# Optimization experiments

Measured on AMD Instinct MI355X. Metric: run time of the kernel, lower is better.

The kernel has to match this reference:

```python
import jax, jax.numpy as jnp
import numpy as np
from jax import lax

FEAT = 56  # features_size
SR = 2     # sr_ratio
NUM_HEADS = 8

# Constant relative-distance indices, shape (N, N, 2) with values in [0, 2*FEAT-2]
_idx = np.array([[i, j] for i in range(FEAT) for j in range(FEAT)])
REL = jnp.asarray(_idx[None, :, :] - _idx[:, None, :] + FEAT - 1)  # (N, N, 2)


def setup_inputs() -> dict:
    key = jax.random.key(0)
    ks = jax.random.split(key, 8)
    dim = 256
    B = 4
    x = jax.random.normal(ks[0], (B, dim, FEAT, FEAT), dtype=jnp.float32)
    Wq = jax.random.normal(ks[1], (dim, dim), dtype=jnp.float32) * 0.02
    Wkv = jax.random.normal(ks[2], (dim, 2 * dim), dtype=jnp.float32) * 0.02
    sr_w = jax.random.normal(ks[3], (dim, dim, SR, SR), dtype=jnp.float32) * 0.02  # OIHW
    sr_b = jnp.zeros((dim,), dtype=jnp.float32)
    ln_g = jnp.ones((dim,), dtype=jnp.float32)
    ln_b = jnp.zeros((dim,), dtype=jnp.float32)
    pos_emb = jax.random.normal(ks[4], (2 * FEAT - 1, 2 * FEAT - 1), dtype=jnp.float32) * 0.2
    proj_w = jax.random.normal(ks[5], (dim, dim), dtype=jnp.float32) * 0.02
    proj_b = jnp.zeros((dim,), dtype=jnp.float32)
    return {"x": x, "Wq": Wq, "Wkv": Wkv, "sr_w": sr_w, "sr_b": sr_b,
            "ln_g": ln_g, "ln_b": ln_b, "pos_emb": pos_emb,
            "proj_w": proj_w, "proj_b": proj_b}


def reference(x, Wq, Wkv, sr_w, sr_b, ln_g, ln_b, pos_emb, proj_w, proj_b):
    B, C, H, W = x.shape
    N = H * W
    h = NUM_HEADS
    hd = C // h
    scale = hd ** -0.5

    x_q = x.reshape(B, C, N).transpose(0, 2, 1)            # (B, N, C)
    q = (x_q @ Wq).reshape(B, N, h, hd).transpose(0, 2, 1, 3)  # (B, h, N, hd)

    # spatial reduction conv (kernel=stride=SR) + layernorm
    xr = lax.conv_general_dilated(x, sr_w, (SR, SR), 'VALID',
                                  dimension_numbers=('NCHW', 'OIHW', 'NCHW'))
    xr = xr + sr_b[None, :, None, None]
    Nk = (H // SR) * (W // SR)
    x_kv = xr.reshape(B, C, Nk).transpose(0, 2, 1)          # (B, Nk, C)
    mu = jnp.mean(x_kv, axis=-1, keepdims=True)
    var = jnp.var(x_kv, axis=-1, keepdims=True)
    x_kv = (x_kv - mu) * lax.rsqrt(var + 1e-5) * ln_g + ln_b

    # kv projection; einops '(dim h l)' split: head_dim slowest, l fastest
    kv = (x_kv @ Wkv).reshape(B, Nk, hd, h, 2)
    k = kv[..., 0].transpose(0, 3, 1, 2)                    # (B, h, Nk, hd)
    v = kv[..., 1].transpose(0, 3, 1, 2)                    # (B, h, Nk, hd)

    attn = jnp.einsum('bhnd,bhmd->bhnm', q, k) * scale      # (B, h, N, Nk)
    bias = pos_emb[REL[..., 0], REL[..., 1]][:, :Nk]        # (N, Nk)
    attn = jax.nn.softmax(attn + bias, axis=-1)

    out = jnp.einsum('bhnm,bhmd->bhnd', attn, v)            # (B, h, N, hd)
    out = out.transpose(0, 2, 1, 3).reshape(B, N, C)
    out = out @ proj_w + proj_b
    return out.transpose(0, 2, 1).reshape(B, C, H, W)
```

## Files before the change

### kernel.cpp

```cpp
#include <hip/hip_runtime.h>
#include <hip/hip_bf16.h>

typedef float f32x4 __attribute__((ext_vector_type(4)));
typedef short s16x8 __attribute__((ext_vector_type(8)));
typedef unsigned short u16x4 __attribute__((ext_vector_type(4)));
typedef unsigned short u16x8 __attribute__((ext_vector_type(8)));

#define MFMA16(a,b,c) __builtin_amdgcn_mfma_f32_16x16x32_bf16(a,b,c,0,0,0)

#define NTOK 3136
#define NKV  784
#define NKVP 800
#define CD   256
#define NH   8
#define HD   32
#define PEW  111
#define LOG2E 1.4426950408889634f
#define SC2  (0.17677669529663687f * 1.4426950408889634f)

static __device__ __forceinline__ unsigned short f2b(float f){
  unsigned int u = __float_as_uint(f);
  return (unsigned short)((u + 0x7fffu + ((u>>16)&1u)) >> 16);
}
static __device__ __forceinline__ unsigned short f2b_fast(float f){
  __hip_bfloat16 h = __float2bfloat16(f);
  return *reinterpret_cast<unsigned short*>(&h);
}
static __device__ __forceinline__ float b2f(unsigned short u){
  return __uint_as_float(((unsigned int)u)<<16);
}
static __device__ __forceinline__ void gload16(const unsigned short* g, unsigned short* l){
  __builtin_amdgcn_global_load_lds(
      (const __attribute__((address_space(1))) unsigned int*)g,
      (__attribute__((address_space(3))) unsigned int*)l, 16, 0, 0);
}

__global__ __launch_bounds__(256) void k_prep(
      const float* __restrict__ Wq, const float* __restrict__ Wkv,
      const float* __restrict__ pw, const float* __restrict__ srw,
      const float* __restrict__ pos, const float* __restrict__ x,
      unsigned short* __restrict__ WqT, unsigned short* __restrict__ WkvT,
      unsigned short* __restrict__ pwT, unsigned short* __restrict__ srwb2,
      unsigned short* __restrict__ bias2, unsigned short* __restrict__ xbf,
      unsigned short* __restrict__ kb, unsigned short* __restrict__ vT){
  __shared__ float tile[64][65];
  const int blk = blockIdx.x, t = threadIdx.x;
  if (blk < 2048){
    int i = blk*256 + t;
    if (i < 65536){ int nn=i>>8, kk=i&255; WqT[i] = f2b(Wq[kk*256+nn]); }
    else if (i < 196608){ int j=i-65536; int c2=j>>8, kk=j&255; WkvT[j] = f2b(Wkv[kk*512+c2]); }
    else if (i < 262144){ int j=i-196608; int cc=j>>8, kk=j&255; pwT[j] = f2b(pw[kk*256+cc]); }
    else { int j=i-262144; int o=j>>10, rem=j&1023, khw=rem>>8, ci=rem&255;
           srwb2[j] = f2b(srw[o*1024 + ci*4 + khw]); }
  } else if (blk < 2176){
    int i = (blk-2048)*256 + t;
    if (i < 16384){
      int bh=i>>9, r=i&511, ridx=r>>5, d=r&31;
      int row = 776 + (ridx&7) + (ridx>>3)*16;
      kb[((size_t)bh*NKVP + row)*HD + d] = 0;
    } else {
      int j=i-16384;
      int bh=j>>9, r=j&511, d=r>>4, key=784+(r&15);
      vT[((size_t)bh*HD + d)*NKVP + key] = 0;
    }
  } else if (blk < 5312){
    int n = blk - 2176;
    if (t < 200){
      int nr = (n*9363)>>19, nc = n - nr*56;
      u16x4 o;
#pragma unroll
      for (int j=0;j<4;++j){
        int key = t*4 + j;
        float v;
        if (key < NKV){
          int tt = (key*9363)>>19, mm = key - tt*56;
          v = pos[(tt-nr+55)*PEW + (mm-nc+55)] * LOG2E;
        } else v = -100000.f;
        o[j] = f2b(v);
      }
      *(u16x4*)&bias2[(size_t)n*NKVP + t*4] = o;
    }
  } else {
    int bx = blk - 5312;
    const int n0 = (bx%49)*64; int c4 = bx/49;
    const int c0 = (c4&3)*64, b = c4>>2;
    const int tx = t&15, ty = t>>4;
#pragma unroll
    for (int j=0;j<4;++j){
      f32x4 v = *(const f32x4*)&x[(size_t)(b*CD + c0+ty+j*16)*NTOK + n0 + tx*4];
      tile[ty+j*16][tx*4+0]=v[0]; tile[ty+j*16][tx*4+1]=v[1];
      tile[ty+j*16][tx*4+2]=v[2]; tile[ty+j*16][tx*4+3]=v[3];
    }
    __syncthreads();
    const int nr = t>>2, ccb = (t&3)*16;
    u16x8 o0, o1;
#pragma unroll
    for (int u=0;u<8;++u){ o0[u] = f2b(tile[ccb+u][nr]); o1[u] = f2b(tile[ccb+8+u][nr]); }
    unsigned short* dst = &xbf[((size_t)b*NTOK + n0+nr)*CD + c0 + ccb];
    *(u16x8*)dst = o0;
    *(u16x8*)(dst+8) = o1;
  }
}

__global__ __launch_bounds__(256) void k_qproj(const unsigned short* __restrict__ xbf,
      const unsigned short* __restrict__ WqT, unsigned short* __restrict__ qb){
  const int tid=threadIdx.x, wv=tid>>6, l=tid&63, g=l>>4, ln16=l&15;
  const int bI = blockIdx.x/49;
  const int n0 = (blockIdx.x%49)*64;
  const int m0 = n0 + (wv>>1)*32;
  const int c0 = blockIdx.y*64 + (wv&1)*32;
  const unsigned short* ap0 = &xbf[((size_t)bI*NTOK + m0+ln16)*CD + g*8];
  const unsigned short* ap1 = ap0 + 16*CD;
  const unsigned short* bp0 = &WqT[(size_t)(c0+ln16)*CD + g*8];
  const unsigned short* bp1 = bp0 + 16*CD;
  f32x4 acc[2][2] = {};
  s16x8 a0 = *(const s16x8*)ap0, a1 = *(const s16x8*)ap1;
  s16x8 w0 = *(const s16x8*)bp0, w1 = *(const s16x8*)bp1;
#pragma unroll
  for (int k0=0; k0<CD; k0+=32){
    s16x8 na0 = *(const s16x8*)(ap0 + k0+32);
    s16x8 na1 = *(const s16x8*)(ap1 + k0+32);
    s16x8 nw0 = *(const s16x8*)(bp0 + k0+32);
    s16x8 nw1 = *(const s16x8*)(bp1 + k0+32);
    acc[0][0] = MFMA16(a0, w0, acc[0][0]);
    acc[0][1] = MFMA16(a0, w1, acc[0][1]);
    acc[1][0] = MFMA16(a1, w0, acc[1][0]);
    acc[1][1] = MFMA16(a1, w1, acc[1][1]);
    a0=na0; a1=na1; w0=nw0; w1=nw1;
  }
#pragma unroll
  for (int mi=0;mi<2;++mi)
#pragma unroll
    for (int ni=0;ni<2;++ni){
      int c = c0 + ni*16 + ln16;
#pragma unroll
      for (int r=0;r<4;++r){
        int n = m0 + mi*16 + g*4 + r;
        qb[((size_t)bI*NTOK + n)*CD + c] = f2b(acc[mi][ni][r] * SC2);
      }
    }
}

__global__ __launch_bounds__(256) void k_conv(const unsigned short* __restrict__ xbf,
      const unsigned short* __restrict__ srwb2, const float* __restrict__ srb,
      float* __restrict__ convo){
  const int tid=threadIdx.x, wv=tid>>6, l=tid&63, g=l>>4, ln16=l&15;
  const int m0 = blockIdx.x*64 + (wv>>1)*32;
  const int c0 = blockIdx.y*64 + (wv&1)*32;
  size_t abase[2][4];
#pragma unroll
  for (int mi=0;mi<2;++mi){
    int m = m0 + mi*16 + ln16;
    int bb = (m>=2352)?3:(m>=1568)?2:(m>=784)?1:0;
    int nk = m - bb*784;
    int pp = (nk*9363)>>18, qq = nk - pp*28;
#pragma unroll
    for (int khw=0;khw<4;++khw){
      int kh = khw>>1, kw = khw&1;
      abase[mi][khw] = ((size_t)bb*NTOK + (2*pp+kh)*56 + 2*qq+kw)*CD;
    }
  }
  const unsigned short* wp0 = &srwb2[(size_t)(c0+ln16)*1024 + g*8];
  const unsigned short* wp1 = wp0 + 16*1024;
  f32x4 acc[2][2] = {};
  s16x8 a0 = *(const s16x8*)&xbf[abase[0][0] + g*8];
  s16x8 a1 = *(const s16x8*)&xbf[abase[1][0] + g*8];
  s16x8 w0 = *(const s16x8*)wp0;
  s16x8 w1 = *(const s16x8*)wp1;
#pragma unroll
  for (int s=0; s<32; ++s){
    const int s1 = s+1;
    const int khw2 = (s1>>3)&3, kc2 = (s1&7)*32;
    const int woff = (s1&31)*32;
    s16x8 na0 = *(const s16x8*)&xbf[abase[0][khw2] + kc2 + g*8];
    s16x8 na1 = *(const s16x8*)&xbf[abase[1][khw2] + kc2 + g*8];
    s16x8 nw0 = *(const s16x8*)(wp0 + woff);
    s16x8 nw1 = *(const s16x8*)(wp1 + woff);
    acc[0][0] = MFMA16(a0, w0, acc[0][0]);
    acc[0][1] = MFMA16(a0, w1, acc[0][1]);
    acc[1][0] = MFMA16(a1, w0, acc[1][0]);
    acc[1][1] = MFMA16(a1, w1, acc[1][1]);
    a0=na0; a1=na1; w0=nw0; w1=nw1;
  }
#pragma unroll
  for (int mi=0;mi<2;++mi)
#pragma unroll
    for (int ni=0;ni<2;++ni){
      int c = c0 + ni*16 + ln16;
      float bias = srb[c];
#pragma unroll
      for (int r=0;r<4;++r){
        int m = m0 + mi*16 + g*4 + r;
        convo[(size_t)m*CD + c] = acc[mi][ni][r] + bias;
      }
    }
}

__global__ void k_ln(const float* __restrict__ co, const float* __restrict__ gam,
                     const float* __restrict__ bet, unsigned short* __restrict__ kvbf){
  const int row = blockIdx.x, t = threadIdx.x;
  float v = co[(size_t)row*CD + t];
  float s = v, s2 = v*v;
#pragma unroll
  for (int o=32; o>0; o>>=1){ s += __shfl_down(s,o); s2 += __shfl_down(s2,o); }
  __shared__ float ps[4], ps2[4];
  int wid = t>>6, lane = t&63;
  if (lane==0){ ps[wid]=s; ps2[wid]=s2; }
  __syncthreads();
  if (t==0){
    float a = ps[0]+ps[1]+ps[2]+ps[3];
    float a2 = ps2[0]+ps2[1]+ps2[2]+ps2[3];
    float mu = a*(1.f/CD);
    float var = a2*(1.f/CD) - mu*mu;
    ps[0] = mu; ps2[0] = rsqrtf(var + 1e-5f);
  }
  __syncthreads();
  float mu = ps[0], rs = ps2[0];
  kvbf[(size_t)row*CD + t] = f2b((v-mu)*rs*gam[t] + bet[t]);
}

__global__ __launch_bounds__(256) void k_kv(const unsigned short* __restrict__ kvbf,
      const unsigned short* __restrict__ WkvT, unsigned short* __restrict__ kb,
      unsigned short* __restrict__ vT){
  const int tid=threadIdx.x, wv=tid>>6, l=tid&63, g=l>>4, ln16=l&15;
  const int m0 = blockIdx.x*64 + (wv>>1)*32;
  const int c0 = blockIdx.y*64 + (wv&1)*32;
  const unsigned short* ap0 = &kvbf[(size_t)(m0+ln16)*CD + g*8];
  const unsigned short* ap1 = ap0 + 16*CD;
  const unsigned short* bp0 = &WkvT[(size_t)(c0+ln16)*CD + g*8];
  const unsigned short* bp1 = bp0 + 16*CD;
  f32x4 acc[2][2] = {};
  s16x8 a0 = *(const s16x8*)ap0, a1 = *(const s16x8*)ap1;
  s16x8 w0 = *(const s16x8*)bp0, w1 = *(const s16x8*)bp1;
#pragma unroll
  for (int k0=0; k0<CD; k0+=32){
    s16x8 na0 = *(const s16x8*)(ap0 + k0+32);
    s16x8 na1 = *(const s16x8*)(ap1 + k0+32);
    s16x8 nw0 = *(const s16x8*)(bp0 + k0+32);
    s16x8 nw1 = *(const s16x8*)(bp1 + k0+32);
    acc[0][0] = MFMA16(a0, w0, acc[0][0]);
    acc[0][1] = MFMA16(a0, w1, acc[0][1]);
    acc[1][0] = MFMA16(a1, w0, acc[1][0]);
    acc[1][1] = MFMA16(a1, w1, acc[1][1]);
    a0=na0; a1=na1; w0=nw0; w1=nw1;
  }
#pragma unroll
  for (int mi=0;mi<2;++mi)
#pragma unroll
    for (int ni=0;ni<2;++ni){
      int c2 = c0 + ni*16 + ln16;
      int d = c2>>4, hh = (c2>>1)&7;
#pragma unroll
      for (int r=0;r<4;++r){
        int m = m0 + mi*16 + g*4 + r;
        int bq = (m>=2352)?3:(m>=1568)?2:(m>=784)?1:0;
        int nk = m - bq*784;
        unsigned short val = f2b(acc[mi][ni][r]);
        if (c2&1){
          vT[(((size_t)bq*NH+hh)*HD + d)*NKVP + nk] = val;
        } else {
          int chunk = nk & ~31, pos = nk & 31;
          int gg = pos>>3, jj = pos&7;
          int row = (jj<4) ? (gg*4+jj) : (16 + gg*4 + (jj-4));
          kb[(((size_t)bq*NH+hh)*NKVP + chunk + row)*HD + d] = val;
        }
      }
    }
}

__global__ __launch_bounds__(256) void k_attn(const unsigned short* __restrict__ qb,
      const unsigned short* __restrict__ kb, const unsigned short* __restrict__ vT,
      const unsigned short* __restrict__ bias2, unsigned short* __restrict__ aout){
  __shared__ unsigned short kv0[2048], kv1[2048], kv2[2048];
  const int tid=threadIdx.x, wv=tid>>6, l=tid&63, g=l>>4, ln16=l&15;
  const int bh = blockIdx.x, b = bh>>3, h = bh&7;
  const int nw = blockIdx.y*64 + wv*16;
  const s16x8 qf = *(const s16x8*)&qb[((size_t)b*NTOK + nw + ln16)*CD + h*HD + g*8];
  const unsigned short* kbase = kb + (size_t)bh*NKVP*HD;
  const unsigned short* vbase = vT + (size_t)bh*HD*NKVP;
  const unsigned short* bp = bias2 + (size_t)(nw + ln16)*NKVP + g*8;
  const int lslot = ((l&3)^((l>>3)&3))*8;
  const unsigned short* sp = (wv < 2)
      ? (kbase + (size_t)(wv*16 + (l>>2))*HD + lslot)
      : (vbase + (size_t)((wv-2)*16 + (l>>2))*NKVP + lslot);
  const int sstep = (wv < 2) ? 1024 : 32;
  const int ko0 = ln16*32 + (g ^ ((ln16>>1)&3))*8;
  unsigned short *bA = kv0, *bB = kv1, *bC = kv2;
  f32x4 accO0 = {}, accO1 = {};
  float S = 0.f;
  const f32x4 zf = {};
  gload16(sp,          bA + wv*512);
  u16x8 bb = *(const u16x8*)bp;
  gload16(sp + sstep,  bB + wv*512);
  u16x8 b1 = *(const u16x8*)(bp + 32);
  for (int it=0; it<25; ++it){
    if (it < 23) asm volatile("s_waitcnt vmcnt(2)" ::: "memory");
    else         asm volatile("s_waitcnt vmcnt(0)" ::: "memory");
    __builtin_amdgcn_s_barrier();
    __builtin_amdgcn_sched_barrier(0);
    u16x8 b2 = b1;
    if (it < 23){
      gload16(sp + (it+2)*sstep, bC + wv*512);
      b2 = *(const u16x8*)(bp + (it+2)*32);
    }
    s16x8 ka0 = *(const s16x8*)&bA[ko0];
    s16x8 ka1 = *(const s16x8*)&bA[512 + ko0];
    s16x8 v0  = *(const s16x8*)&bA[1024 + ko0];
    s16x8 v1  = *(const s16x8*)&bA[1536 + ko0];
    __builtin_amdgcn_s_setprio(1);
    f32x4 d0 = MFMA16(ka0, qf, zf);
    f32x4 d1 = MFMA16(ka1, qf, zf);
    float p[8];
#pragma unroll
    for (int r=0;r<4;++r){
      p[r]   = exp2f(d0[r] + b2f(bb[r]));
      p[4+r] = exp2f(d1[r] + b2f(bb[4+r]));
    }
    S += ((p[0]+p[1])+(p[2]+p[3])) + ((p[4]+p[5])+(p[6]+p[7]));
    s16x8 pf;
#pragma unroll
    for (int j=0;j<8;++j) pf[j] = (short)f2b_fast(p[j]);
    accO0 = MFMA16(pf, v0, accO0);
    accO1 = MFMA16(pf, v1, accO1);
    __builtin_amdgcn_s_setprio(0);
    unsigned short* tmp = bA; bA = bB; bB = bC; bC = tmp;
    bb = b1; b1 = b2;
  }
  S += __shfl_xor(S, 16);
  S += __shfl_xor(S, 32);
#pragma unroll
  for (int r=0;r<4;++r){
    float Sr = __shfl(S, g*4 + r);
    float inv = 1.f / Sr;
    int n = nw + g*4 + r;
    aout[((size_t)b*NTOK + n)*CD + h*HD + ln16]      = f2b(accO0[r]*inv);
    aout[((size_t)b*NTOK + n)*CD + h*HD + 16 + ln16] = f2b(accO1[r]*inv);
  }
}

__global__ __launch_bounds__(256) void k_proj(const unsigned short* __restrict__ ain,
      const unsigned short* __restrict__ pwT, const float* __restrict__ pb,
      float* __restrict__ out){
  const int tid=threadIdx.x, wv=tid>>6, l=tid&63, g=l>>4, ln16=l&15;
  const int bI = blockIdx.x/49;
  const int n0 = (blockIdx.x%49)*64;
  const int nsub = n0 + (wv&1)*32;
  const int c0 = blockIdx.y*64 + (wv>>1)*32;
  const unsigned short* ap0 = &pwT[(size_t)(c0+ln16)*CD + g*8];
  const unsigned short* ap1 = ap0 + 16*CD;
  const unsigned short* bp0 = &ain[((size_t)bI*NTOK + nsub+ln16)*CD + g*8];
  const unsigned short* bp1 = bp0 + 16*CD;
  f32x4 acc[2][2] = {};
  s16x8 a0 = *(const s16x8*)ap0, a1 = *(const s16x8*)ap1;
  s16x8 w0 = *(const s16x8*)bp0, w1 = *(const s16x8*)bp1;
#pragma unroll
  for (int k0=0; k0<CD; k0+=32){
    s16x8 na0 = *(const s16x8*)(ap0 + k0+32);
    s16x8 na1 = *(const s16x8*)(ap1 + k0+32);
    s16x8 nw0 = *(const s16x8*)(bp0 + k0+32);
    s16x8 nw1 = *(const s16x8*)(bp1 + k0+32);
    acc[0][0] = MFMA16(a0, w0, acc[0][0]);
    acc[0][1] = MFMA16(a0, w1, acc[0][1]);
    acc[1][0] = MFMA16(a1, w0, acc[1][0]);
    acc[1][1] = MFMA16(a1, w1, acc[1][1]);
    a0=na0; a1=na1; w0=nw0; w1=nw1;
  }
#pragma unroll
  for (int mi=0;mi<2;++mi)
#pragma unroll
    for (int r=0;r<4;++r){
      int c = c0 + mi*16 + g*4 + r;
      float bias = pb[c];
#pragma unroll
      for (int ni=0;ni<2;++ni){
        int n = nsub + ni*16 + ln16;
        out[((size_t)bI*CD + c)*NTOK + n] = acc[mi][ni][r] + bias;
      }
    }
}

extern "C" void kernel_launch(void* const* d_in, const int* in_sizes, int n_in,
                              void* d_out, int out_size, void* d_ws, size_t ws_size,
                              hipStream_t stream){
  const float* x   = (const float*)d_in[0];
  const float* Wq  = (const float*)d_in[1];
  const float* Wkv = (const float*)d_in[2];
  const float* srw = (const float*)d_in[3];
  const float* srb = (const float*)d_in[4];
  const float* lng = (const float*)d_in[5];
  const float* lnb = (const float*)d_in[6];
  const float* pos = (const float*)d_in[7];
  const float* pw  = (const float*)d_in[8];
  const float* pb  = (const float*)d_in[9];
  float* out = (float*)d_out;

  unsigned char* p = (unsigned char*)d_ws;
  unsigned short* WqT   = (unsigned short*)(p + 0);
  unsigned short* WkvT  = (unsigned short*)(p + 131072);
  unsigned short* pwT   = (unsigned short*)(p + 393216);
  unsigned short* srwb2 = (unsigned short*)(p + 524288);
  unsigned short* bias2 = (unsigned short*)(p + 1048576);
  unsigned short* xbf   = (unsigned short*)(p + 6066176);
  unsigned short* qbuf  = (unsigned short*)(p + 12488704);
  float*          convo = (float*)        (p + 18911232);
  unsigned short* kvbf  = (unsigned short*)(p + 22122496);
  unsigned short* kbuf  = (unsigned short*)(p + 23728128);
  unsigned short* vT    = (unsigned short*)(p + 25366528);
  unsigned short* aout  = (unsigned short*)(p + 27004928);

  k_prep <<<6096, 256, 0, stream>>>(Wq, Wkv, pw, srw, pos, x,
                                    WqT, WkvT, pwT, srwb2, bias2, xbf, kbuf, vT);
  k_qproj<<<dim3(196,4), 256, 0, stream>>>(xbf, WqT, qbuf);
  k_conv <<<dim3(49,4),  256, 0, stream>>>(xbf, srwb2, srb, convo);
  k_ln   <<<3136, 256, 0, stream>>>(convo, lng, lnb, kvbf);
  k_kv   <<<dim3(49,8),  256, 0, stream>>>(kvbf, WkvT, kbuf, vT);
  k_attn <<<dim3(32,49), 256, 0, stream>>>(qbuf, kbuf, vT, bias2, aout);
  k_proj <<<dim3(196,4), 256, 0, stream>>>(aout, pwT, pb, out);
}
```

Before: 193.4 us.

## Fuse kernels, tile weight transposes, and process two query tiles per attention block

The Q projection and the spatial-reduction conv now run as one launch sharing a grid. LayerNorm is fused into the KV projection through a swizzled LDS tile, which removes the intermediate bf16 buffer and one launch. Weight transposes in prep go through an LDS-tiled path for coalesced access. The attention kernel handles two 64-row query tiles per block so each staged K/V tile is reused twice, and it packs probabilities to bf16 with a cheaper rounding. The costs are higher register pressure in attention, a masked tail tile, and the LayerNorm now being recomputed by each of the 8 column blocks.

```diff
diff --git a/kernel.cpp b/kernel.cpp
--- a/kernel.cpp
+++ b/kernel.cpp
@@ -22,10 +22,6 @@
   unsigned int u = __float_as_uint(f);
   return (unsigned short)((u + 0x7fffu + ((u>>16)&1u)) >> 16);
 }
-static __device__ __forceinline__ unsigned short f2b_fast(float f){
-  __hip_bfloat16 h = __float2bfloat16(f);
-  return *reinterpret_cast<unsigned short*>(&h);
-}
 static __device__ __forceinline__ float b2f(unsigned short u){
   return __uint_as_float(((unsigned int)u)<<16);
 }
@@ -33,6 +29,18 @@
   __builtin_amdgcn_global_load_lds(
       (const __attribute__((address_space(1))) unsigned int*)g,
       (__attribute__((address_space(3))) unsigned int*)l, 16, 0, 0);
+}
+static __device__ __forceinline__ s16x8 pack8(const float* p){
+  union { uint4 u; s16x8 s; } w;
+  unsigned int a0=__float_as_uint(p[0])+0x8000u, a1=__float_as_uint(p[1])+0x8000u;
+  unsigned int a2=__float_as_uint(p[2])+0x8000u, a3=__float_as_uint(p[3])+0x8000u;
+  unsigned int a4=__float_as_uint(p[4])+0x8000u, a5=__float_as_uint(p[5])+0x8000u;
+  unsigned int a6=__float_as_uint(p[6])+0x8000u, a7=__float_as_uint(p[7])+0x8000u;
+  w.u.x = (a0>>16) | (a1 & 0xFFFF0000u);
+  w.u.y = (a2>>16) | (a3 & 0xFFFF0000u);
+  w.u.z = (a4>>16) | (a5 & 0xFFFF0000u);
+  w.u.w = (a6>>16) | (a7 & 0xFFFF0000u);
+  return w.s;
 }
 
 __global__ __launch_bounds__(256) void k_prep(
@@ -45,15 +53,32 @@
       unsigned short* __restrict__ kb, unsigned short* __restrict__ vT){
   __shared__ float tile[64][65];
   const int blk = blockIdx.x, t = threadIdx.x;
-  if (blk < 2048){
-    int i = blk*256 + t;
-    if (i < 65536){ int nn=i>>8, kk=i&255; WqT[i] = f2b(Wq[kk*256+nn]); }
-    else if (i < 196608){ int j=i-65536; int c2=j>>8, kk=j&255; WkvT[j] = f2b(Wkv[kk*512+c2]); }
-    else if (i < 262144){ int j=i-196608; int cc=j>>8, kk=j&255; pwT[j] = f2b(pw[kk*256+cc]); }
-    else { int j=i-262144; int o=j>>10, rem=j&1023, khw=rem>>8, ci=rem&255;
-           srwb2[j] = f2b(srw[o*1024 + ci*4 + khw]); }
-  } else if (blk < 2176){
-    int i = (blk-2048)*256 + t;
+  const int tx = t&15, ty = t>>4;
+  if (blk < 64){
+    const float* src; unsigned short* dst; int sr0, sc0, sstr;
+    if (blk < 16){ src=Wq; dst=WqT; sstr=256; sr0=(blk>>2)*64; sc0=(blk&3)*64; }
+    else if (blk < 32){ int b2=blk-16; src=pw; dst=pwT; sstr=256; sr0=(b2>>2)*64; sc0=(b2&3)*64; }
+    else { int b2=blk-32; src=Wkv; dst=WkvT; sstr=512; sr0=(b2>>3)*64; sc0=(b2&7)*64; }
+#pragma unroll
+    for (int j=0;j<4;++j){
+      f32x4 v = *(const f32x4*)&src[(size_t)(sr0+ty+j*16)*sstr + sc0 + tx*4];
+      tile[ty+j*16][tx*4+0]=v[0]; tile[ty+j*16][tx*4+1]=v[1];
+      tile[ty+j*16][tx*4+2]=v[2]; tile[ty+j*16][tx*4+3]=v[3];
+    }
+    __syncthreads();
+    const int nr = t>>2, ccb = (t&3)*16;
+    u16x8 o0, o1;
+#pragma unroll
+    for (int u=0;u<8;++u){ o0[u]=f2b(tile[ccb+u][nr]); o1[u]=f2b(tile[ccb+8+u][nr]); }
+    unsigned short* dp = &dst[(size_t)(sc0+nr)*256 + sr0 + ccb];
+    *(u16x8*)dp = o0;
+    *(u16x8*)(dp+8) = o1;
+  } else if (blk < 1088){
+    int j = (blk-64)*256 + t;
+    int o=j>>10, rem=j&1023, khw=rem>>8, ci=rem&255;
+    srwb2[j] = f2b(srw[o*1024 + ci*4 + khw]);
+  } else if (blk < 1216){
+    int i = (blk-1088)*256 + t;
     if (i < 16384){
       int bh=i>>9, r=i&511, ridx=r>>5, d=r&31;
       int row = 776 + (ridx&7) + (ridx>>3)*16;
@@ -63,10 +88,10 @@
       int bh=j>>9, r=j&511, d=r>>4, key=784+(r&15);
       vT[((size_t)bh*HD + d)*NKVP + key] = 0;
     }
-  } else if (blk < 5312){
-    int n = blk - 2176;
+  } else if (blk < 4352){
+    int n = blk - 1216;
     if (t < 200){
-      int nr = (n*9363)>>19, nc = n - nr*56;
+      int nr2 = (n*9363)>>19, nc = n - nr2*56;
       u16x4 o;
 #pragma unroll
       for (int j=0;j<4;++j){
@@ -74,17 +99,16 @@
         float v;
         if (key < NKV){
           int tt = (key*9363)>>19, mm = key - tt*56;
-          v = pos[(tt-nr+55)*PEW + (mm-nc+55)] * LOG2E;
+          v = pos[(tt-nr2+55)*PEW + (mm-nc+55)] * LOG2E;
         } else v = -100000.f;
         o[j] = f2b(v);
       }
       *(u16x4*)&bias2[(size_t)n*NKVP + t*4] = o;
     }
   } else {
-    int bx = blk - 5312;
+    int bx = blk - 4352;
     const int n0 = (bx%49)*64; int c4 = bx/49;
     const int c0 = (c4&3)*64, b = c4>>2;
-    const int tx = t&15, ty = t>>4;
 #pragma unroll
     for (int j=0;j<4;++j){
       f32x4 v = *(const f32x4*)&x[(size_t)(b*CD + c0+ty+j*16)*NTOK + n0 + tx*4];
@@ -95,154 +119,169 @@
     const int nr = t>>2, ccb = (t&3)*16;
     u16x8 o0, o1;
 #pragma unroll
-    for (int u=0;u<8;++u){ o0[u] = f2b(tile[ccb+u][nr]); o1[u] = f2b(tile[ccb+8+u][nr]); }
+    for (int u=0;u<8;++u){ o0[u]=f2b(tile[ccb+u][nr]); o1[u]=f2b(tile[ccb+8+u][nr]); }
     unsigned short* dst = &xbf[((size_t)b*NTOK + n0+nr)*CD + c0 + ccb];
     *(u16x8*)dst = o0;
     *(u16x8*)(dst+8) = o1;
   }
 }
 
-__global__ __launch_bounds__(256) void k_qproj(const unsigned short* __restrict__ xbf,
-      const unsigned short* __restrict__ WqT, unsigned short* __restrict__ qb){
+__global__ __launch_bounds__(256) void k_qc(const unsigned short* __restrict__ xbf,
+      const unsigned short* __restrict__ WqT, const unsigned short* __restrict__ srwb2,
+      const float* __restrict__ srb, unsigned short* __restrict__ qb,
+      float* __restrict__ convo){
+  const int gid = blockIdx.x;
   const int tid=threadIdx.x, wv=tid>>6, l=tid&63, g=l>>4, ln16=l&15;
-  const int bI = blockIdx.x/49;
-  const int n0 = (blockIdx.x%49)*64;
-  const int m0 = n0 + (wv>>1)*32;
+  if (gid < 784){
+    const int bx = gid % 196, by = gid / 196;
+    const int bI = bx/49;
+    const int n0 = (bx%49)*64;
+    const int m0 = n0 + (wv>>1)*32;
+    const int c0 = by*64 + (wv&1)*32;
+    const unsigned short* ap0 = &xbf[((size_t)bI*NTOK + m0+ln16)*CD + g*8];
+    const unsigned short* ap1 = ap0 + 16*CD;
+    const unsigned short* bp0 = &WqT[(size_t)(c0+ln16)*CD + g*8];
+    const unsigned short* bp1 = bp0 + 16*CD;
+    f32x4 acc[2][2] = {};
+    s16x8 a0 = *(const s16x8*)ap0, a1 = *(const s16x8*)ap1;
+    s16x8 w0 = *(const s16x8*)bp0, w1 = *(const s16x8*)bp1;
+#pragma unroll
+    for (int k0=0; k0<CD; k0+=32){
+      s16x8 na0 = *(const s16x8*)(ap0 + k0+32);
+      s16x8 na1 = *(const s16x8*)(ap1 + k0+32);
+      s16x8 nw0 = *(const s16x8*)(bp0 + k0+32);
+      s16x8 nw1 = *(const s16x8*)(bp1 + k0+32);
+      acc[0][0] = MFMA16(a0, w0, acc[0][0]);
+      acc[0][1] = MFMA16(a0, w1, acc[0][1]);
+      acc[1][0] = MFMA16(a1, w0, acc[1][0]);
+      acc[1][1] = MFMA16(a1, w1, acc[1][1]);
+      a0=na0; a1=na1; w0=nw0; w1=nw1;
+    }
+#pragma unroll
+    for (int mi=0;mi<2;++mi)
+#pragma unroll
+      for (int ni=0;ni<2;++ni){
+        int c = c0 + ni*16 + ln16;
+#pragma unroll
+        for (int r=0;r<4;++r){
+          int n = m0 + mi*16 + g*4 + r;
+          qb[((size_t)bI*NTOK + n)*CD + c] = f2b(acc[mi][ni][r] * SC2);
+        }
+      }
+  } else {
+    const int cid = gid - 784;
+    const int m0 = (cid%49)*64 + (wv>>1)*32;
+    const int c0 = (cid/49)*64 + (wv&1)*32;
+    size_t abase[2][4];
+#pragma unroll
+    for (int mi=0;mi<2;++mi){
+      int m = m0 + mi*16 + ln16;
+      int bb = (m>=2352)?3:(m>=1568)?2:(m>=784)?1:0;
+      int nk = m - bb*784;
+      int pp = (nk*9363)>>18, qq = nk - pp*28;
+#pragma unroll
+      for (int khw=0;khw<4;++khw){
+        int kh = khw>>1, kw = khw&1;
+        abase[mi][khw] = ((size_t)bb*NTOK + (2*pp+kh)*56 + 2*qq+kw)*CD;
+      }
+    }
+    const unsigned short* wp0 = &srwb2[(size_t)(c0+ln16)*1024 + g*8];
+    const unsigned short* wp1 = wp0 + 16*1024;
+    f32x4 acc[2][2] = {};
+    s16x8 a0 = *(const s16x8*)&xbf[abase[0][0] + g*8];
+    s16x8 a1 = *(const s16x8*)&xbf[abase[1][0] + g*8];
+    s16x8 w0 = *(const s16x8*)wp0;
+    s16x8 w1 = *(const s16x8*)wp1;
+#pragma unroll
+    for (int s=0; s<32; ++s){
+      const int s1 = s+1;
+      const int khw2 = (s1>>3)&3, kc2 = (s1&7)*32;
+      const int woff = (s1&31)*32;
+      s16x8 na0 = *(const s16x8*)&xbf[abase[0][khw2] + kc2 + g*8];
+      s16x8 na1 = *(const s16x8*)&xbf[abase[1][khw2] + kc2 + g*8];
+      s16x8 nw0 = *(const s16x8*)(wp0 + woff);
+      s16x8 nw1 = *(const s16x8*)(wp1 + woff);
+      acc[0][0] = MFMA16(a0, w0, acc[0][0]);
+      acc[0][1] = MFMA16(a0, w1, acc[0][1]);
+      acc[1][0] = MFMA16(a1, w0, acc[1][0]);
+      acc[1][1] = MFMA16(a1, w1, acc[1][1]);
+      a0=na0; a1=na1; w0=nw0; w1=nw1;
+    }
+#pragma unroll
+    for (int mi=0;mi<2;++mi)
+#pragma unroll
+      for (int ni=0;ni<2;++ni){
+        int c = c0 + ni*16 + ln16;
+        float bias = srb[c];
+#pragma unroll
+        for (int r=0;r<4;++r){
+          int m = m0 + mi*16 + g*4 + r;
+          convo[(size_t)m*CD + c] = acc[mi][ni][r] + bias;
+        }
+      }
+  }
+}
+
+__global__ __launch_bounds__(256) void k_kvln(const float* __restrict__ co,
+      const float* __restrict__ gam, const float* __restrict__ bet,
+      const unsigned short* __restrict__ WkvT, unsigned short* __restrict__ kb,
+      unsigned short* __restrict__ vT){
+  __shared__ unsigned short As[64*256];
+  const int tid=threadIdx.x, wv=tid>>6, l=tid&63, g=l>>4, ln16=l&15;
+  const int m0blk = blockIdx.x*64;
+  {
+    const int rl = tid>>2, cs = (tid&3)*64;
+    const float* src = &co[(size_t)(m0blk+rl)*CD + cs];
+    f32x4 vals[16];
+    float s=0.f, s2=0.f;
+#pragma unroll
+    for (int i=0;i<16;++i){
+      vals[i] = *(const f32x4*)(src + i*4);
+#pragma unroll
+      for (int q=0;q<4;++q){ s += vals[i][q]; s2 += vals[i][q]*vals[i][q]; }
+    }
+    s += __shfl_xor(s,1); s2 += __shfl_xor(s2,1);
+    s += __shfl_xor(s,2); s2 += __shfl_xor(s2,2);
+    float mu = s*(1.f/CD);
+    float rs = rsqrtf(s2*(1.f/CD) - mu*mu + 1e-5f);
+#pragma unroll
+    for (int u=0;u<8;++u){
+      f32x4 g4a = *(const f32x4*)&gam[cs+u*8];
+      f32x4 g4b = *(const f32x4*)&gam[cs+u*8+4];
+      f32x4 b4a = *(const f32x4*)&bet[cs+u*8];
+      f32x4 b4b = *(const f32x4*)&bet[cs+u*8+4];
+      u16x8 o;
+#pragma unroll
+      for (int q=0;q<4;++q){
+        o[q]   = f2b((vals[u*2][q]  -mu)*rs*g4a[q] + b4a[q]);
+        o[4+q] = f2b((vals[u*2+1][q]-mu)*rs*g4b[q] + b4b[q]);
+      }
+      int off = (rl*256 + cs + u*8) ^ ((rl&7)<<3);
+      *(u16x8*)&As[off] = o;
+    }
+  }
+  __syncthreads();
+  const int mw0 = (wv>>1)*32;
   const int c0 = blockIdx.y*64 + (wv&1)*32;
-  const unsigned short* ap0 = &xbf[((size_t)bI*NTOK + m0+ln16)*CD + g*8];
-  const unsigned short* ap1 = ap0 + 16*CD;
-  const unsigned short* bp0 = &WqT[(size_t)(c0+ln16)*CD + g*8];
+  const unsigned short* bp0 = &WkvT[(size_t)(c0+ln16)*CD + g*8];
   const unsigned short* bp1 = bp0 + 16*CD;
   f32x4 acc[2][2] = {};
-  s16x8 a0 = *(const s16x8*)ap0, a1 = *(const s16x8*)ap1;
   s16x8 w0 = *(const s16x8*)bp0, w1 = *(const s16x8*)bp1;
+  const int mr0 = mw0 + ln16, mr1 = mw0 + 16 + ln16;
 #pragma unroll
   for (int k0=0; k0<CD; k0+=32){
-    s16x8 na0 = *(const s16x8*)(ap0 + k0+32);
-    s16x8 na1 = *(const s16x8*)(ap1 + k0+32);
-    s16x8 nw0 = *(const s16x8*)(bp0 + k0+32);
-    s16x8 nw1 = *(const s16x8*)(bp1 + k0+32);
+    s16x8 a0 = *(const s16x8*)&As[(mr0*256 + k0 + g*8) ^ ((mr0&7)<<3)];
+    s16x8 a1 = *(const s16x8*)&As[(mr1*256 + k0 + g*8) ^ ((mr1&7)<<3)];
+    s16x8 nw0 = w0, nw1 = w1;
+    if (k0 < CD-32){
+      nw0 = *(const s16x8*)(bp0 + k0+32);
+      nw1 = *(const s16x8*)(bp1 + k0+32);
+    }
     acc[0][0] = MFMA16(a0, w0, acc[0][0]);
     acc[0][1] = MFMA16(a0, w1, acc[0][1]);
     acc[1][0] = MFMA16(a1, w0, acc[1][0]);
     acc[1][1] = MFMA16(a1, w1, acc[1][1]);
-    a0=na0; a1=na1; w0=nw0; w1=nw1;
-  }
-#pragma unroll
-  for (int mi=0;mi<2;++mi)
-#pragma unroll
-    for (int ni=0;ni<2;++ni){
-      int c = c0 + ni*16 + ln16;
-#pragma unroll
-      for (int r=0;r<4;++r){
-        int n = m0 + mi*16 + g*4 + r;
-        qb[((size_t)bI*NTOK + n)*CD + c] = f2b(acc[mi][ni][r] * SC2);
-      }
-    }
-}
-
-__global__ __launch_bounds__(256) void k_conv(const unsigned short* __restrict__ xbf,
-      const unsigned short* __restrict__ srwb2, const float* __restrict__ srb,
-      float* __restrict__ convo){
-  const int tid=threadIdx.x, wv=tid>>6, l=tid&63, g=l>>4, ln16=l&15;
-  const int m0 = blockIdx.x*64 + (wv>>1)*32;
-  const int c0 = blockIdx.y*64 + (wv&1)*32;
-  size_t abase[2][4];
-#pragma unroll
-  for (int mi=0;mi<2;++mi){
-    int m = m0 + mi*16 + ln16;
-    int bb = (m>=2352)?3:(m>=1568)?2:(m>=784)?1:0;
-    int nk = m - bb*784;
-    int pp = (nk*9363)>>18, qq = nk - pp*28;
-#pragma unroll
-    for (int khw=0;khw<4;++khw){
-      int kh = khw>>1, kw = khw&1;
-      abase[mi][khw] = ((size_t)bb*NTOK + (2*pp+kh)*56 + 2*qq+kw)*CD;
-    }
-  }
-  const unsigned short* wp0 = &srwb2[(size_t)(c0+ln16)*1024 + g*8];
-  const unsigned short* wp1 = wp0 + 16*1024;
-  f32x4 acc[2][2] = {};
-  s16x8 a0 = *(const s16x8*)&xbf[abase[0][0] + g*8];
-  s16x8 a1 = *(const s16x8*)&xbf[abase[1][0] + g*8];
-  s16x8 w0 = *(const s16x8*)wp0;
-  s16x8 w1 = *(const s16x8*)wp1;
-#pragma unroll
-  for (int s=0; s<32; ++s){
-    const int s1 = s+1;
-    const int khw2 = (s1>>3)&3, kc2 = (s1&7)*32;
-    const int woff = (s1&31)*32;
-    s16x8 na0 = *(const s16x8*)&xbf[abase[0][khw2] + kc2 + g*8];
-    s16x8 na1 = *(const s16x8*)&xbf[abase[1][khw2] + kc2 + g*8];
-    s16x8 nw0 = *(const s16x8*)(wp0 + woff);
-    s16x8 nw1 = *(const s16x8*)(wp1 + woff);
-    acc[0][0] = MFMA16(a0, w0, acc[0][0]);
-    acc[0][1] = MFMA16(a0, w1, acc[0][1]);
-    acc[1][0] = MFMA16(a1, w0, acc[1][0]);
-    acc[1][1] = MFMA16(a1, w1, acc[1][1]);
-    a0=na0; a1=na1; w0=nw0; w1=nw1;
-  }
-#pragma unroll
-  for (int mi=0;mi<2;++mi)
-#pragma unroll
-    for (int ni=0;ni<2;++ni){
-      int c = c0 + ni*16 + ln16;
-      float bias = srb[c];
-#pragma unroll
-      for (int r=0;r<4;++r){
-        int m = m0 + mi*16 + g*4 + r;
-        convo[(size_t)m*CD + c] = acc[mi][ni][r] + bias;
-      }
-    }
-}
-
-__global__ void k_ln(const float* __restrict__ co, const float* __restrict__ gam,
-                     const float* __restrict__ bet, unsigned short* __restrict__ kvbf){
-  const int row = blockIdx.x, t = threadIdx.x;
-  float v = co[(size_t)row*CD + t];
-  float s = v, s2 = v*v;
-#pragma unroll
-  for (int o=32; o>0; o>>=1){ s += __shfl_down(s,o); s2 += __shfl_down(s2,o); }
-  __shared__ float ps[4], ps2[4];
-  int wid = t>>6, lane = t&63;
-  if (lane==0){ ps[wid]=s; ps2[wid]=s2; }
-  __syncthreads();
-  if (t==0){
-    float a = ps[0]+ps[1]+ps[2]+ps[3];
-    float a2 = ps2[0]+ps2[1]+ps2[2]+ps2[3];
-    float mu = a*(1.f/CD);
-    float var = a2*(1.f/CD) - mu*mu;
-    ps[0] = mu; ps2[0] = rsqrtf(var + 1e-5f);
-  }
-  __syncthreads();
-  float mu = ps[0], rs = ps2[0];
-  kvbf[(size_t)row*CD + t] = f2b((v-mu)*rs*gam[t] + bet[t]);
-}
-
-__global__ __launch_bounds__(256) void k_kv(const unsigned short* __restrict__ kvbf,
-      const unsigned short* __restrict__ WkvT, unsigned short* __restrict__ kb,
-      unsigned short* __restrict__ vT){
-  const int tid=threadIdx.x, wv=tid>>6, l=tid&63, g=l>>4, ln16=l&15;
-  const int m0 = blockIdx.x*64 + (wv>>1)*32;
-  const int c0 = blockIdx.y*64 + (wv&1)*32;
-  const unsigned short* ap0 = &kvbf[(size_t)(m0+ln16)*CD + g*8];
-  const unsigned short* ap1 = ap0 + 16*CD;
-  const unsigned short* bp0 = &WkvT[(size_t)(c0+ln16)*CD + g*8];
-  const unsigned short* bp1 = bp0 + 16*CD;
-  f32x4 acc[2][2] = {};
-  s16x8 a0 = *(const s16x8*)ap0, a1 = *(const s16x8*)ap1;
-  s16x8 w0 = *(const s16x8*)bp0, w1 = *(const s16x8*)bp1;
-#pragma unroll
-  for (int k0=0; k0<CD; k0+=32){
-    s16x8 na0 = *(const s16x8*)(ap0 + k0+32);
-    s16x8 na1 = *(const s16x8*)(ap1 + k0+32);
-    s16x8 nw0 = *(const s16x8*)(bp0 + k0+32);
-    s16x8 nw1 = *(const s16x8*)(bp1 + k0+32);
-    acc[0][0] = MFMA16(a0, w0, acc[0][0]);
-    acc[0][1] = MFMA16(a0, w1, acc[0][1]);
-    acc[1][0] = MFMA16(a1, w0, acc[1][0]);
-    acc[1][1] = MFMA16(a1, w1, acc[1][1]);
-    a0=na0; a1=na1; w0=nw0; w1=nw1;
+    w0=nw0; w1=nw1;
   }
 #pragma unroll
   for (int mi=0;mi<2;++mi)
@@ -252,7 +291,7 @@
       int d = c2>>4, hh = (c2>>1)&7;
 #pragma unroll
       for (int r=0;r<4;++r){
-        int m = m0 + mi*16 + g*4 + r;
+        int m = m0blk + mw0 + mi*16 + g*4 + r;
         int bq = (m>=2352)?3:(m>=1568)?2:(m>=784)?1:0;
         int nk = m - bq*784;
         unsigned short val = f2b(acc[mi][ni][r]);
@@ -274,11 +313,16 @@
   __shared__ unsigned short kv0[2048], kv1[2048], kv2[2048];
   const int tid=threadIdx.x, wv=tid>>6, l=tid&63, g=l>>4, ln16=l&15;
   const int bh = blockIdx.x, b = bh>>3, h = bh&7;
-  const int nw = blockIdx.y*64 + wv*16;
-  const s16x8 qf = *(const s16x8*)&qb[((size_t)b*NTOK + nw + ln16)*CD + h*HD + g*8];
+  const int nq0 = blockIdx.y*128 + wv*16;
+  const int nq1 = nq0 + 64;
+  const bool act1 = (nq1 < NTOK);
+  const int nq1c = act1 ? nq1 : nq0;
+  const s16x8 qf0 = *(const s16x8*)&qb[((size_t)b*NTOK + nq0  + ln16)*CD + h*HD + g*8];
+  const s16x8 qf1 = *(const s16x8*)&qb[((size_t)b*NTOK + nq1c + ln16)*CD + h*HD + g*8];
   const unsigned short* kbase = kb + (size_t)bh*NKVP*HD;
   const unsigned short* vbase = vT + (size_t)bh*HD*NKVP;
-  const unsigned short* bp = bias2 + (size_t)(nw + ln16)*NKVP + g*8;
+  const unsigned short* bp0 = bias2 + (size_t)(nq0  + ln16)*NKVP + g*8;
+  const unsigned short* bp1 = bias2 + (size_t)(nq1c + ln16)*NKVP + g*8;
   const int lslot = ((l&3)^((l>>3)&3))*8;
   const unsigned short* sp = (wv < 2)
       ? (kbase + (size_t)(wv*16 + (l>>2))*HD + lslot)
@@ -286,55 +330,73 @@
   const int sstep = (wv < 2) ? 1024 : 32;
   const int ko0 = ln16*32 + (g ^ ((ln16>>1)&3))*8;
   unsigned short *bA = kv0, *bB = kv1, *bC = kv2;
-  f32x4 accO0 = {}, accO1 = {};
-  float S = 0.f;
+  f32x4 acc00={}, acc01={}, acc10={}, acc11={};
+  float S0=0.f, S1=0.f;
   const f32x4 zf = {};
-  gload16(sp,          bA + wv*512);
-  u16x8 bb = *(const u16x8*)bp;
-  gload16(sp + sstep,  bB + wv*512);
-  u16x8 b1 = *(const u16x8*)(bp + 32);
+  gload16(sp, bA + wv*512);
+  u16x8 bb0 = *(const u16x8*)bp0;
+  u16x8 bb1 = *(const u16x8*)bp1;
+  gload16(sp + sstep, bB + wv*512);
+  u16x8 c0v = *(const u16x8*)(bp0 + 32);
+  u16x8 c1v = *(const u16x8*)(bp1 + 32);
   for (int it=0; it<25; ++it){
-    if (it < 23) asm volatile("s_waitcnt vmcnt(2)" ::: "memory");
+    if (it < 23) asm volatile("s_waitcnt vmcnt(3)" ::: "memory");
     else         asm volatile("s_waitcnt vmcnt(0)" ::: "memory");
     __builtin_amdgcn_s_barrier();
     __builtin_amdgcn_sched_barrier(0);
-    u16x8 b2 = b1;
+    u16x8 n0v = c0v, n1v = c1v;
     if (it < 23){
       gload16(sp + (it+2)*sstep, bC + wv*512);
-      b2 = *(const u16x8*)(bp + (it+2)*32);
+      n0v = *(const u16x8*)(bp0 + (it+2)*32);
+      n1v = *(const u16x8*)(bp1 + (it+2)*32);
     }
     s16x8 ka0 = *(const s16x8*)&bA[ko0];
     s16x8 ka1 = *(const s16x8*)&bA[512 + ko0];
     s16x8 v0  = *(const s16x8*)&bA[1024 + ko0];
     s16x8 v1  = *(const s16x8*)&bA[1536 + ko0];
     __builtin_amdgcn_s_setprio(1);
-    f32x4 d0 = MFMA16(ka0, qf, zf);
-    f32x4 d1 = MFMA16(ka1, qf, zf);
-    float p[8];
+    f32x4 d00 = MFMA16(ka0, qf0, zf);
+    f32x4 d10 = MFMA16(ka1, qf0, zf);
+    f32x4 d01 = MFMA16(ka0, qf1, zf);
+    f32x4 d11 = MFMA16(ka1, qf1, zf);
+    float p0[8], p1[8];
 #pragma unroll
     for (int r=0;r<4;++r){
-      p[r]   = exp2f(d0[r] + b2f(bb[r]));
-      p[4+r] = exp2f(d1[r] + b2f(bb[4+r]));
-    }
-    S += ((p[0]+p[1])+(p[2]+p[3])) + ((p[4]+p[5])+(p[6]+p[7]));
-    s16x8 pf;
-#pragma unroll
-    for (int j=0;j<8;++j) pf[j] = (short)f2b_fast(p[j]);
-    accO0 = MFMA16(pf, v0, accO0);
-    accO1 = MFMA16(pf, v1, accO1);
+      p0[r]   = exp2f(d00[r] + b2f(bb0[r]));
+      p0[4+r] = exp2f(d10[r] + b2f(bb0[4+r]));
+      p1[r]   = exp2f(d01[r] + b2f(bb1[r]));
+      p1[4+r] = exp2f(d11[r] + b2f(bb1[4+r]));
+    }
+    S0 += ((p0[0]+p0[1])+(p0[2]+p0[3])) + ((p0[4]+p0[5])+(p0[6]+p0[7]));
+    S1 += ((p1[0]+p1[1])+(p1[2]+p1[3])) + ((p1[4]+p1[5])+(p1[6]+p1[7]));
+    s16x8 pf0 = pack8(p0);
+    s16x8 pf1 = pack8(p1);
+    acc00 = MFMA16(pf0, v0, acc00);
+    acc01 = MFMA16(pf0, v1, acc01);
+    acc10 = MFMA16(pf1, v0, acc10);
+    acc11 = MFMA16(pf1, v1, acc11);
     __builtin_amdgcn_s_setprio(0);
     unsigned short* tmp = bA; bA = bB; bB = bC; bC = tmp;
-    bb = b1; b1 = b2;
-  }
-  S += __shfl_xor(S, 16);
-  S += __shfl_xor(S, 32);
+    bb0 = c0v; c0v = n0v;
+    bb1 = c1v; c1v = n1v;
+  }
+  S0 += __shfl_xor(S0, 16); S0 += __shfl_xor(S0, 32);
+  S1 += __shfl_xor(S1, 16); S1 += __shfl_xor(S1, 32);
 #pragma unroll
   for (int r=0;r<4;++r){
-    float Sr = __shfl(S, g*4 + r);
-    float inv = 1.f / Sr;
-    int n = nw + g*4 + r;
-    aout[((size_t)b*NTOK + n)*CD + h*HD + ln16]      = f2b(accO0[r]*inv);
-    aout[((size_t)b*NTOK + n)*CD + h*HD + 16 + ln16] = f2b(accO1[r]*inv);
+    float inv = 1.f / __shfl(S0, g*4 + r);
+    int n = nq0 + g*4 + r;
+    aout[((size_t)b*NTOK + n)*CD + h*HD + ln16]      = f2b(acc00[r]*inv);
+    aout[((size_t)b*NTOK + n)*CD + h*HD + 16 + ln16] = f2b(acc01[r]*inv);
+  }
+  if (act1){
+#pragma unroll
+    for (int r=0;r<4;++r){
+      float inv = 1.f / __shfl(S1, g*4 + r);
+      int n = nq1 + g*4 + r;
+      aout[((size_t)b*NTOK + n)*CD + h*HD + ln16]      = f2b(acc10[r]*inv);
+      aout[((size_t)b*NTOK + n)*CD + h*HD + 16 + ln16] = f2b(acc11[r]*inv);
+    }
   }
 }
 
@@ -403,17 +465,14 @@
   unsigned short* xbf   = (unsigned short*)(p + 6066176);
   unsigned short* qbuf  = (unsigned short*)(p + 12488704);
   float*          convo = (float*)        (p + 18911232);
-  unsigned short* kvbf  = (unsigned short*)(p + 22122496);
-  unsigned short* kbuf  = (unsigned short*)(p + 23728128);
-  unsigned short* vT    = (unsigned short*)(p + 25366528);
-  unsigned short* aout  = (unsigned short*)(p + 27004928);
-
-  k_prep <<<6096, 256, 0, stream>>>(Wq, Wkv, pw, srw, pos, x,
+  unsigned short* kbuf  = (unsigned short*)(p + 22122496);
+  unsigned short* vT    = (unsigned short*)(p + 23760896);
+  unsigned short* aout  = (unsigned short*)(p + 25399296);
+
+  k_prep <<<5136, 256, 0, stream>>>(Wq, Wkv, pw, srw, pos, x,
                                     WqT, WkvT, pwT, srwb2, bias2, xbf, kbuf, vT);
-  k_qproj<<<dim3(196,4), 256, 0, stream>>>(xbf, WqT, qbuf);
-  k_conv <<<dim3(49,4),  256, 0, stream>>>(xbf, srwb2, srb, convo);
-  k_ln   <<<3136, 256, 0, stream>>>(convo, lng, lnb, kvbf);
-  k_kv   <<<dim3(49,8),  256, 0, stream>>>(kvbf, WkvT, kbuf, vT);
-  k_attn <<<dim3(32,49), 256, 0, stream>>>(qbuf, kbuf, vT, bias2, aout);
+  k_qc   <<<980, 256, 0, stream>>>(xbf, WqT, srwb2, srb, qbuf, convo);
+  k_kvln <<<dim3(49,8), 256, 0, stream>>>(convo, lng, lnb, WkvT, kbuf, vT);
+  k_attn <<<dim3(32,25), 256, 0, stream>>>(qbuf, kbuf, vT, bias2, aout);
   k_proj <<<dim3(196,4), 256, 0, stream>>>(aout, pwT, pb, out);
 }
```

Result: slower. 200.1 us (+3.5%).
